# Kernel optimization log

Measured on AMD Instinct MI355X. Metric: run time of the kernel, lower is better.

Reference implementation:

```python
import jax, jax.numpy as jnp
import numpy as np

TOP_K = 2
NUM_EXPERTS = 64
TEMPERATURE = 3.0           # buffer initial value (moe_routing_temperature default)
LOAD_BALANCE_ALPHA = 0.01
Z_LOSS_ALPHA = 1e-4


def setup_inputs() -> dict:
    key = jax.random.key(0)
    k1, k2 = jax.random.split(key)
    B, S, H, E = 4, 4096, 4096, NUM_EXPERTS
    x = jax.random.normal(k1, (B, S, H), dtype=jnp.float32)
    gate_w = jax.random.normal(k2, (E, H), dtype=jnp.float32) * (1.0 / np.sqrt(H))
    expert_bias = jnp.zeros((E,), dtype=jnp.float32)
    return {"x": x, "gate_w": gate_w, "expert_bias": expert_bias}


def reference(x, gate_w, expert_bias):
    # Eval-mode path: no noise, no warmup scaling, static top_k, seq_len < 8192
    # -> logits scaled by the temperature buffer.
    B, S, H = x.shape
    E = gate_w.shape[0]
    x_flat = x.reshape(-1, H)                               # [T, H], T = B*S
    logits = jnp.einsum('th,eh->te', x_flat, gate_w) + expert_bias  # [T, E]
    logits = logits / TEMPERATURE
    probs = jax.nn.softmax(logits, axis=-1)                 # [T, E]
    top_scores, top_idx = jax.lax.top_k(probs, TOP_K)       # [T, K]
    top_scores = top_scores / jnp.sum(top_scores, axis=-1, keepdims=True)
    # Load-balance aux loss: fraction of routed tokens per expert * mean prob.
    sel_counts = jax.nn.one_hot(top_idx, E, dtype=logits.dtype).sum(axis=1)  # [T, E]
    frac_routed = sel_counts.mean(axis=0)                   # [E], sums to TOP_K
    mean_prob = probs.mean(axis=0)                          # [E]
    lb_loss = LOAD_BALANCE_ALPHA * E * jnp.sum(frac_routed * mean_prob)
    # Z-loss for routing stability.
    z_loss = Z_LOSS_ALPHA * jnp.mean(jax.nn.logsumexp(logits, axis=-1) ** 2)
    total_loss = lb_loss + z_loss
    return top_scores, top_idx, total_loss
```

## Files before the change

kernel.cpp:

```cpp
#include <hip/hip_runtime.h>
#include <hip/hip_bf16.h>
#include <math.h>

typedef float f32x4 __attribute__((ext_vector_type(4)));

#define H_DIM   4096
#define E_EXP   64
#define NTOK    16384
#define BT      64
#define BK      64
#define LDX     68
#define NBLK    (NTOK/BT)
#define PART_STRIDE 132

__global__ __launch_bounds__(256) void moe_gate_main(
    const float* __restrict__ x, const float* __restrict__ gw,
    const float* __restrict__ bias, float* __restrict__ out,
    float* __restrict__ part)
{
    __shared__ float xs[BT * LDX];
    __shared__ float ws[E_EXP * LDX];
    __shared__ float bs[E_EXP];
    __shared__ float rs[BT];
    __shared__ int   ia[BT], ib[BT];

    const int tid  = threadIdx.x;
    const int bid  = blockIdx.x;
    const int tok0 = bid * BT;
    const int tx   = tid & 15;
    const int ty   = tid >> 4;

    if (tid < E_EXP) bs[tid] = bias[tid];

    const int srow = tid >> 4;
    const int scol = (tid & 15) * 4;
    const float* xp = x  + (size_t)(tok0 + srow) * H_DIM + scol;
    const float* wp = gw + (size_t)srow * H_DIM + scol;

    float acc[4][4];
#pragma unroll
    for (int i = 0; i < 4; i++)
#pragma unroll
        for (int j = 0; j < 4; j++) acc[i][j] = 0.f;

    f32x4 rx[4], rw[4];
#pragma unroll
    for (int i = 0; i < 4; i++) {
        rx[i] = *(const f32x4*)(xp + (size_t)(16 * i) * H_DIM);
        rw[i] = *(const f32x4*)(wp + (size_t)(16 * i) * H_DIM);
    }

    for (int c = 0; c < H_DIM / BK; c++) {
        __syncthreads();
#pragma unroll
        for (int i = 0; i < 4; i++) {
            *(f32x4*)&xs[(srow + 16 * i) * LDX + scol] = rx[i];
            *(f32x4*)&ws[(srow + 16 * i) * LDX + scol] = rw[i];
        }
        __syncthreads();
        if (c + 1 < H_DIM / BK) {
            const int k0 = (c + 1) * BK;
#pragma unroll
            for (int i = 0; i < 4; i++) {
                rx[i] = *(const f32x4*)(xp + (size_t)(16 * i) * H_DIM + k0);
                rw[i] = *(const f32x4*)(wp + (size_t)(16 * i) * H_DIM + k0);
            }
        }
#pragma unroll
        for (int kk = 0; kk < BK; kk += 4) {
            f32x4 xv[4], wv[4];
#pragma unroll
            for (int i = 0; i < 4; i++) xv[i] = *(const f32x4*)&xs[(ty + 16 * i) * LDX + kk];
#pragma unroll
            for (int j = 0; j < 4; j++) wv[j] = *(const f32x4*)&ws[(tx + 16 * j) * LDX + kk];
#pragma unroll
            for (int i = 0; i < 4; i++)
#pragma unroll
                for (int j = 0; j < 4; j++)
#pragma unroll
                    for (int q = 0; q < 4; q++)
                        acc[i][j] += xv[i][q] * wv[j][q];
        }
    }

    __syncthreads();
#pragma unroll
    for (int i = 0; i < 4; i++)
#pragma unroll
        for (int j = 0; j < 4; j++)
            xs[(ty + 16 * i) * LDX + (tx + 16 * j)] = acc[i][j];
    __syncthreads();

    float zsq = 0.f;
    if (tid < BT) {
        const float invTemp = (1.0f / 3.0f);
        float m = -1e30f, m2 = -1e30f;
        int i1 = 0, i2 = 0;
        for (int e = 0; e < E_EXP; e++) {
            float v = (xs[tid * LDX + e] + bs[e]) * invTemp;
            xs[tid * LDX + e] = v;
            if (v > m)       { m2 = m; i2 = i1; m = v; i1 = e; }
            else if (v > m2) { m2 = v; i2 = e; }
        }
        float s = 0.f;
        for (int e = 0; e < E_EXP; e++) {
            float p = expf(xs[tid * LDX + e] - m);
            xs[tid * LDX + e] = p;
            s += p;
        }
        rs[tid] = 1.0f / s;
        ia[tid] = i1; ib[tid] = i2;

        float p2   = expf(m2 - m);
        float inv12 = 1.0f / (1.0f + p2);
        out[(size_t)(tok0 + tid) * 2 + 0] = inv12;
        out[(size_t)(tok0 + tid) * 2 + 1] = p2 * inv12;
        out[(size_t)NTOK * 2 + (size_t)(tok0 + tid) * 2 + 0] = (float)i1;
        out[(size_t)NTOK * 2 + (size_t)(tok0 + tid) * 2 + 1] = (float)i2;

        float lse = m + logf(s);
        zsq = lse * lse;
#pragma unroll
        for (int o = 32; o; o >>= 1) zsq += __shfl_xor(zsq, o);
    }
    __syncthreads();

    if (tid < E_EXP) {
        float psum = 0.f, csum = 0.f;
        for (int t = 0; t < BT; t++) {
            psum += xs[t * LDX + tid] * rs[t];
            csum += (ia[t] == tid ? 1.f : 0.f) + (ib[t] == tid ? 1.f : 0.f);
        }
        part[bid * PART_STRIDE + tid]      = psum;
        part[bid * PART_STRIDE + 64 + tid] = csum;
        if (tid == 0) part[bid * PART_STRIDE + 128] = zsq;
    }
}

__global__ void moe_gate_loss(const float* __restrict__ part, float* __restrict__ out)
{
    const int tid = threadIdx.x;
    float sp = 0.f, sc = 0.f, zp = 0.f;
    for (int b = 0; b < NBLK; b++) {
        sp += part[b * PART_STRIDE + tid];
        sc += part[b * PART_STRIDE + 64 + tid];
    }
    for (int m = 0; m < NBLK / 64; m++)
        zp += part[(tid + 64 * m) * PART_STRIDE + 128];

    const float invN = 1.0f / (float)NTOK;
    float dot = (sc * invN) * (sp * invN);
#pragma unroll
    for (int o = 32; o; o >>= 1) {
        dot += __shfl_xor(dot, o);
        zp  += __shfl_xor(zp, o);
    }
    if (tid == 0)
        out[(size_t)NTOK * 4] = 0.01f * 64.0f * dot + 1e-4f * zp * invN;
}

extern "C" void kernel_launch(void* const* d_in, const int* in_sizes, int n_in,
                              void* d_out, int out_size, void* d_ws, size_t ws_size,
                              hipStream_t stream)
{
    const float* x    = (const float*)d_in[0];
    const float* gw   = (const float*)d_in[1];
    const float* bias = (const float*)d_in[2];
    float* out  = (float*)d_out;
    float* part = (float*)d_ws;

    moe_gate_main<<<NBLK, 256, 0, stream>>>(x, gw, bias, out, part);
    moe_gate_loss<<<1, 64, 0, stream>>>(part, out);
}
```

Measured before the change: 477.4 us.

## Use split-bf16 MFMA emulation of fp32 GEMM and parallelize loss reduction

Replaces the FP32 FMA tiled GEMM with bf16 MFMA instructions, splitting each fp32 value into three bf16 parts and summing six cross products to keep close to fp32 accuracy. The weights are converted and double-buffered in shared memory, while each wave reads its x rows directly from global memory into registers. The aim is to remove the scalar FMA compute bound. It costs extra conversion ALU work per element and some small precision change. The final loss kernel is also widened to 1024 threads with a shared-memory reduction instead of a serial 64-thread loop.

```diff
diff --git a/kernel.cpp b/kernel.cpp
--- a/kernel.cpp
+++ b/kernel.cpp
@@ -3,115 +3,166 @@
 #include <math.h>
 
 typedef float f32x4 __attribute__((ext_vector_type(4)));
-
-#define H_DIM   4096
-#define E_EXP   64
-#define NTOK    16384
-#define BT      64
-#define BK      64
-#define LDX     68
-#define NBLK    (NTOK/BT)
-#define PART_STRIDE 132
+typedef short bf16x8 __attribute__((ext_vector_type(8)));
+
+#define H_DIM 4096
+#define E_EXP 64
+#define NTOK  16384
+#define NCH   128
+#define WSTR  40
+#define PS    132
+#define NBLK  256
+
+__device__ __forceinline__ unsigned rne16(float v){
+    unsigned u = __float_as_uint(v);
+    return (u + 0x7fffu + ((u >> 16) & 1u)) >> 16;
+}
+__device__ __forceinline__ float fromb16(unsigned s){ return __uint_as_float(s << 16); }
+
+__device__ __forceinline__ void split8(f32x4 a, f32x4 b, bf16x8 &h, bf16x8 &m, bf16x8 &l){
+#pragma unroll
+    for (int j = 0; j < 8; j++){
+        float v = (j < 4) ? a[j] : b[j - 4];
+        unsigned hu = rne16(v);  float r1 = v  - fromb16(hu);
+        unsigned mu = rne16(r1); float r2 = r1 - fromb16(mu);
+        unsigned lu = rne16(r2);
+        h[j] = (short)hu; m[j] = (short)mu; l[j] = (short)lu;
+    }
+}
+
+#define MFMA __builtin_amdgcn_mfma_f32_16x16x32_bf16
 
 __global__ __launch_bounds__(256) void moe_gate_main(
     const float* __restrict__ x, const float* __restrict__ gw,
     const float* __restrict__ bias, float* __restrict__ out,
     float* __restrict__ part)
 {
-    __shared__ float xs[BT * LDX];
-    __shared__ float ws[E_EXP * LDX];
-    __shared__ float bs[E_EXP];
-    __shared__ float rs[BT];
-    __shared__ int   ia[BT], ib[BT];
-
-    const int tid  = threadIdx.x;
-    const int bid  = blockIdx.x;
-    const int tok0 = bid * BT;
-    const int tx   = tid & 15;
-    const int ty   = tid >> 4;
-
-    if (tid < E_EXP) bs[tid] = bias[tid];
-
-    const int srow = tid >> 4;
-    const int scol = (tid & 15) * 4;
-    const float* xp = x  + (size_t)(tok0 + srow) * H_DIM + scol;
-    const float* wp = gw + (size_t)srow * H_DIM + scol;
-
-    float acc[4][4];
-#pragma unroll
-    for (int i = 0; i < 4; i++)
-#pragma unroll
-        for (int j = 0; j < 4; j++) acc[i][j] = 0.f;
-
-    f32x4 rx[4], rw[4];
-#pragma unroll
-    for (int i = 0; i < 4; i++) {
-        rx[i] = *(const f32x4*)(xp + (size_t)(16 * i) * H_DIM);
-        rw[i] = *(const f32x4*)(wp + (size_t)(16 * i) * H_DIM);
-    }
-
-    for (int c = 0; c < H_DIM / BK; c++) {
+    __shared__ short wbuf[2][3][E_EXP * WSTR];
+    __shared__ float ls[64 * 68];
+    __shared__ float bs[64], rs[64];
+    __shared__ int   ia[64], ib[64];
+
+    const int tid = threadIdx.x, bid = blockIdx.x;
+    const int tok0 = bid * 64;
+    const int wv = tid >> 6, l = tid & 63, l16 = l & 15, lk = l >> 4;
+
+    if (tid < 64) bs[tid] = bias[tid];
+
+    const float* xp = x + (size_t)(tok0 + 16 * wv + l16) * H_DIM + lk * 8;
+    const int we = tid >> 2, wk = (tid & 3) * 8;
+    const float* wp = gw + (size_t)we * H_DIM + wk;
+    const int wo_base = we * WSTR + wk;
+
+    f32x4 acc[4] = {};
+
+    f32x4 w0a = *(const f32x4*)(wp);
+    f32x4 w0b = *(const f32x4*)(wp + 4);
+    f32x4 xe0 = *(const f32x4*)(xp);
+    f32x4 xe1 = *(const f32x4*)(xp + 4);
+    f32x4 xo0 = *(const f32x4*)(xp + 32);
+    f32x4 xo1 = *(const f32x4*)(xp + 36);
+    f32x4 wn0 = *(const f32x4*)(wp + 32);
+    f32x4 wn1 = *(const f32x4*)(wp + 36);
+    {
+        bf16x8 h, m, lo; split8(w0a, w0b, h, m, lo);
+        *(bf16x8*)&wbuf[0][0][wo_base] = h;
+        *(bf16x8*)&wbuf[0][1][wo_base] = m;
+        *(bf16x8*)&wbuf[0][2][wo_base] = lo;
+    }
+    __syncthreads();
+
+    for (int cp = 0; cp < 64; cp++){
+        const int c0 = 2 * cp;
+        {
+            bf16x8 xh, xm, xl; split8(xe0, xe1, xh, xm, xl);
+            if (cp < 63){
+                xe0 = *(const f32x4*)(xp + (c0 + 2) * 32);
+                xe1 = *(const f32x4*)(xp + (c0 + 2) * 32 + 4);
+            }
+            {
+                bf16x8 h, m, lo; split8(wn0, wn1, h, m, lo);
+                *(bf16x8*)&wbuf[1][0][wo_base] = h;
+                *(bf16x8*)&wbuf[1][1][wo_base] = m;
+                *(bf16x8*)&wbuf[1][2][wo_base] = lo;
+            }
+            if (cp < 63){
+                wn0 = *(const f32x4*)(wp + (c0 + 2) * 32);
+                wn1 = *(const f32x4*)(wp + (c0 + 2) * 32 + 4);
+            }
+#pragma unroll
+            for (int g = 0; g < 4; g++){
+                const int wo = (g * 16 + l16) * WSTR + lk * 8;
+                bf16x8 wh = *(const bf16x8*)&wbuf[0][0][wo];
+                bf16x8 wm = *(const bf16x8*)&wbuf[0][1][wo];
+                bf16x8 wl = *(const bf16x8*)&wbuf[0][2][wo];
+                acc[g] = MFMA(xh, wh, acc[g], 0, 0, 0);
+                acc[g] = MFMA(xm, wh, acc[g], 0, 0, 0);
+                acc[g] = MFMA(xh, wm, acc[g], 0, 0, 0);
+                acc[g] = MFMA(xm, wm, acc[g], 0, 0, 0);
+                acc[g] = MFMA(xh, wl, acc[g], 0, 0, 0);
+                acc[g] = MFMA(xl, wh, acc[g], 0, 0, 0);
+            }
+        }
         __syncthreads();
-#pragma unroll
-        for (int i = 0; i < 4; i++) {
-            *(f32x4*)&xs[(srow + 16 * i) * LDX + scol] = rx[i];
-            *(f32x4*)&ws[(srow + 16 * i) * LDX + scol] = rw[i];
+        {
+            bf16x8 xh, xm, xl; split8(xo0, xo1, xh, xm, xl);
+            if (cp < 63){
+                xo0 = *(const f32x4*)(xp + (c0 + 3) * 32);
+                xo1 = *(const f32x4*)(xp + (c0 + 3) * 32 + 4);
+            }
+            if (cp < 63){
+                bf16x8 h, m, lo; split8(wn0, wn1, h, m, lo);
+                *(bf16x8*)&wbuf[0][0][wo_base] = h;
+                *(bf16x8*)&wbuf[0][1][wo_base] = m;
+                *(bf16x8*)&wbuf[0][2][wo_base] = lo;
+                wn0 = *(const f32x4*)(wp + (c0 + 3) * 32);
+                wn1 = *(const f32x4*)(wp + (c0 + 3) * 32 + 4);
+            }
+#pragma unroll
+            for (int g = 0; g < 4; g++){
+                const int wo = (g * 16 + l16) * WSTR + lk * 8;
+                bf16x8 wh = *(const bf16x8*)&wbuf[1][0][wo];
+                bf16x8 wm = *(const bf16x8*)&wbuf[1][1][wo];
+                bf16x8 wl = *(const bf16x8*)&wbuf[1][2][wo];
+                acc[g] = MFMA(xh, wh, acc[g], 0, 0, 0);
+                acc[g] = MFMA(xm, wh, acc[g], 0, 0, 0);
+                acc[g] = MFMA(xh, wm, acc[g], 0, 0, 0);
+                acc[g] = MFMA(xm, wm, acc[g], 0, 0, 0);
+                acc[g] = MFMA(xh, wl, acc[g], 0, 0, 0);
+                acc[g] = MFMA(xl, wh, acc[g], 0, 0, 0);
+            }
         }
         __syncthreads();
-        if (c + 1 < H_DIM / BK) {
-            const int k0 = (c + 1) * BK;
-#pragma unroll
-            for (int i = 0; i < 4; i++) {
-                rx[i] = *(const f32x4*)(xp + (size_t)(16 * i) * H_DIM + k0);
-                rw[i] = *(const f32x4*)(wp + (size_t)(16 * i) * H_DIM + k0);
-            }
-        }
-#pragma unroll
-        for (int kk = 0; kk < BK; kk += 4) {
-            f32x4 xv[4], wv[4];
-#pragma unroll
-            for (int i = 0; i < 4; i++) xv[i] = *(const f32x4*)&xs[(ty + 16 * i) * LDX + kk];
-#pragma unroll
-            for (int j = 0; j < 4; j++) wv[j] = *(const f32x4*)&ws[(tx + 16 * j) * LDX + kk];
-#pragma unroll
-            for (int i = 0; i < 4; i++)
-#pragma unroll
-                for (int j = 0; j < 4; j++)
-#pragma unroll
-                    for (int q = 0; q < 4; q++)
-                        acc[i][j] += xv[i][q] * wv[j][q];
-        }
-    }
-
-    __syncthreads();
-#pragma unroll
-    for (int i = 0; i < 4; i++)
-#pragma unroll
-        for (int j = 0; j < 4; j++)
-            xs[(ty + 16 * i) * LDX + (tx + 16 * j)] = acc[i][j];
+    }
+
+#pragma unroll
+    for (int g = 0; g < 4; g++)
+#pragma unroll
+        for (int r = 0; r < 4; r++)
+            ls[(16 * wv + lk * 4 + r) * 68 + g * 16 + l16] = acc[g][r];
     __syncthreads();
 
     float zsq = 0.f;
-    if (tid < BT) {
+    if (tid < 64) {
         const float invTemp = (1.0f / 3.0f);
         float m = -1e30f, m2 = -1e30f;
         int i1 = 0, i2 = 0;
         for (int e = 0; e < E_EXP; e++) {
-            float v = (xs[tid * LDX + e] + bs[e]) * invTemp;
-            xs[tid * LDX + e] = v;
+            float v = (ls[tid * 68 + e] + bs[e]) * invTemp;
+            ls[tid * 68 + e] = v;
             if (v > m)       { m2 = m; i2 = i1; m = v; i1 = e; }
             else if (v > m2) { m2 = v; i2 = e; }
         }
         float s = 0.f;
         for (int e = 0; e < E_EXP; e++) {
-            float p = expf(xs[tid * LDX + e] - m);
-            xs[tid * LDX + e] = p;
+            float p = expf(ls[tid * 68 + e] - m);
+            ls[tid * 68 + e] = p;
             s += p;
         }
         rs[tid] = 1.0f / s;
         ia[tid] = i1; ib[tid] = i2;
 
-        float p2   = expf(m2 - m);
+        float p2    = expf(m2 - m);
         float inv12 = 1.0f / (1.0f + p2);
         out[(size_t)(tok0 + tid) * 2 + 0] = inv12;
         out[(size_t)(tok0 + tid) * 2 + 1] = p2 * inv12;
@@ -127,36 +178,46 @@
 
     if (tid < E_EXP) {
         float psum = 0.f, csum = 0.f;
-        for (int t = 0; t < BT; t++) {
-            psum += xs[t * LDX + tid] * rs[t];
+        for (int t = 0; t < 64; t++) {
+            psum += ls[t * 68 + tid] * rs[t];
             csum += (ia[t] == tid ? 1.f : 0.f) + (ib[t] == tid ? 1.f : 0.f);
         }
-        part[bid * PART_STRIDE + tid]      = psum;
-        part[bid * PART_STRIDE + 64 + tid] = csum;
-        if (tid == 0) part[bid * PART_STRIDE + 128] = zsq;
-    }
-}
-
-__global__ void moe_gate_loss(const float* __restrict__ part, float* __restrict__ out)
+        part[bid * PS + tid]      = psum;
+        part[bid * PS + 64 + tid] = csum;
+        if (tid == 0) part[bid * PS + 128] = zsq;
+    }
+}
+
+__global__ __launch_bounds__(1024) void moe_gate_loss(
+    const float* __restrict__ part, float* __restrict__ out)
 {
+    __shared__ float spS[16][64], scS[16][64], zS[256];
     const int tid = threadIdx.x;
-    float sp = 0.f, sc = 0.f, zp = 0.f;
-    for (int b = 0; b < NBLK; b++) {
-        sp += part[b * PART_STRIDE + tid];
-        sc += part[b * PART_STRIDE + 64 + tid];
-    }
-    for (int m = 0; m < NBLK / 64; m++)
-        zp += part[(tid + 64 * m) * PART_STRIDE + 128];
-
-    const float invN = 1.0f / (float)NTOK;
-    float dot = (sc * invN) * (sp * invN);
-#pragma unroll
-    for (int o = 32; o; o >>= 1) {
-        dot += __shfl_xor(dot, o);
-        zp  += __shfl_xor(zp, o);
-    }
-    if (tid == 0)
-        out[(size_t)NTOK * 4] = 0.01f * 64.0f * dot + 1e-4f * zp * invN;
+    const int e = tid & 63, g = tid >> 6;
+    float sp = 0.f, sc = 0.f;
+    for (int b = g; b < NBLK; b += 16) {
+        sp += part[b * PS + e];
+        sc += part[b * PS + 64 + e];
+    }
+    spS[g][e] = sp; scS[g][e] = sc;
+    if (tid < 256) zS[tid] = part[tid * PS + 128];
+    __syncthreads();
+
+    if (tid < 64) {
+        float tsp = 0.f, tsc = 0.f;
+#pragma unroll
+        for (int g2 = 0; g2 < 16; g2++) { tsp += spS[g2][tid]; tsc += scS[g2][tid]; }
+        float zp = zS[tid] + zS[tid + 64] + zS[tid + 128] + zS[tid + 192];
+        const float invN = 1.0f / (float)NTOK;
+        float dot = (tsc * invN) * (tsp * invN);
+#pragma unroll
+        for (int o = 32; o; o >>= 1) {
+            dot += __shfl_xor(dot, o);
+            zp  += __shfl_xor(zp, o);
+        }
+        if (tid == 0)
+            out[(size_t)NTOK * 4] = 0.01f * 64.0f * dot + 1e-4f * zp * invN;
+    }
 }
 
 extern "C" void kernel_launch(void* const* d_in, const int* in_sizes, int n_in,
@@ -170,5 +231,5 @@
     float* part = (float*)d_ws;
 
     moe_gate_main<<<NBLK, 256, 0, stream>>>(x, gw, bias, out, part);
-    moe_gate_loss<<<1, 64, 0, stream>>>(part, out);
-}
+    moe_gate_loss<<<1, 1024, 0, stream>>>(part, out);
+}
```

Result: no change. 485.3 us (+1.7%).
